# Kernel optimization log

Measured on AMD Instinct MI355X. Metric: run time of the kernel, lower is better.

Reference implementation:

```python
import jax, jax.numpy as jnp
import numpy as np

D_MODEL = 1024
N_EXPERTS = 16
TOP_K = 2
D_FF = 512      # per-expert SwiGLU hidden size
D_FF_SHARED = 1024
N_TOKENS = 4096


def setup_inputs() -> dict:
    key = jax.random.key(0)
    ks = jax.random.split(key, 9)
    s_in = 1.0 / np.sqrt(D_MODEL)
    s_ff = 1.0 / np.sqrt(D_FF)
    s_fs = 1.0 / np.sqrt(D_FF_SHARED)
    return {
        "hidden_states": jax.random.normal(ks[0], (N_TOKENS, D_MODEL), jnp.float32),
        "Wg": jax.random.normal(ks[1], (D_MODEL, N_EXPERTS), jnp.float32) * s_in,
        "w1": jax.random.normal(ks[2], (N_EXPERTS, D_MODEL, D_FF), jnp.float32) * s_in,
        "w3": jax.random.normal(ks[3], (N_EXPERTS, D_MODEL, D_FF), jnp.float32) * s_in,
        "w2": jax.random.normal(ks[4], (N_EXPERTS, D_FF, D_MODEL), jnp.float32) * s_ff,
        "ws1": jax.random.normal(ks[5], (D_MODEL, D_FF_SHARED), jnp.float32) * s_in,
        "ws3": jax.random.normal(ks[6], (D_MODEL, D_FF_SHARED), jnp.float32) * s_in,
        "ws2": jax.random.normal(ks[7], (D_FF_SHARED, D_MODEL), jnp.float32) * s_fs,
        "capacity": 1024,
    }


def reference(hidden_states, Wg, w1, w3, w2, ws1, ws3, ws2, capacity):
    T, d = hidden_states.shape
    E = Wg.shape[1]
    C = capacity

    # --- router: softmax in fp32, top-k, renormalize (norm_topk_prob=True) ---
    logits = hidden_states @ Wg                                  # [T, E]
    probs = jax.nn.softmax(logits.astype(jnp.float32), axis=-1)
    topw, topi = jax.lax.top_k(probs, TOP_K)                     # [T, K]
    topw = topw / jnp.sum(topw, axis=-1, keepdims=True)
    topw = topw.astype(hidden_states.dtype)

    # --- dispatch: flatten (token, k) pairs, compute slot within expert buffer ---
    flat_e = topi.reshape(-1)                                    # [T*K] expert id
    flat_t = jnp.repeat(jnp.arange(T), TOP_K)                    # [T*K] source token
    flat_w = topw.reshape(-1)                                    # [T*K]
    oh = jax.nn.one_hot(flat_e, E, dtype=jnp.int32)              # [T*K, E]
    # exclusive position of each pair within its expert's buffer
    pos = jnp.sum((jnp.cumsum(oh, axis=0) - 1) * oh, axis=-1)    # [T*K]
    keep = pos < C
    slot = jnp.where(keep, flat_e * C + pos, E * C)              # dropped -> dummy row

    buf = jnp.zeros((E * C + 1, d), hidden_states.dtype)
    buf = buf.at[slot].set(hidden_states[flat_t])
    xb = buf[: E * C].reshape(E, C, d)                           # [E, C, d]

    # --- per-expert SwiGLU MLP (grouped matmuls) ---
    h = jax.nn.silu(jnp.einsum("ecd,edf->ecf", xb, w1)) * jnp.einsum("ecd,edf->ecf", xb, w3)
    ob = jnp.einsum("ecf,efd->ecd", h, w2).reshape(E * C, d)     # [E*C, d]

    # --- weighted combine: gather expert outputs, scatter-add into token rows ---
    gathered = ob[jnp.minimum(slot, E * C - 1)]                  # [T*K, d]
    y = gathered * (flat_w * keep.astype(flat_w.dtype))[:, None]
    final = jnp.zeros_like(hidden_states).at[flat_t].add(y)

    # --- shared expert (dense SwiGLU over all tokens) ---
    sh = jax.nn.silu(hidden_states @ ws1) * (hidden_states @ ws3)
    final = final + sh @ ws2
    return final
```

## Files before the change

### kernel.cpp

```cpp
#include <hip/hip_runtime.h>
#include <stdint.h>

#define TT 4096
#define DM 1024
#define NE 16
#define DFF 512
#define DFS 1024
#define CAP 1024

typedef unsigned short u16;
typedef __bf16 bf16x8 __attribute__((ext_vector_type(8)));
typedef float f32x4 __attribute__((ext_vector_type(4)));

typedef __attribute__((address_space(1))) void as1_void;
typedef __attribute__((address_space(3))) void as3_void;

__device__ __forceinline__ u16 f2bf(float f) {
  union { float f; uint32_t u; } v; v.f = f;
  uint32_t u = v.u;
  u += 0x7fffu + ((u >> 16) & 1u);
  return (u16)(u >> 16);
}

__device__ __forceinline__ float bf2f(u16 b) {
  union { uint32_t u; float f; } v; v.u = ((uint32_t)b) << 16;
  return v.f;
}

__device__ __forceinline__ void gl2lds16(const void* g, void* l) {
  __builtin_amdgcn_global_load_lds(
      (as1_void*)(uintptr_t)g,
      (as3_void*)(uint32_t)(uintptr_t)l,
      16, 0, 0);
}

__global__ __launch_bounds__(256) void k_prep(
    const float* __restrict__ x, const float* __restrict__ Wg,
    const float* __restrict__ w1, const float* __restrict__ w3,
    const float* __restrict__ w2, const float* __restrict__ ws1,
    const float* __restrict__ ws3, const float* __restrict__ ws2,
    u16* __restrict__ hbf,
    u16* __restrict__ w1t, u16* __restrict__ w3t, u16* __restrict__ w2t,
    u16* __restrict__ ws1t, u16* __restrict__ ws3t, u16* __restrict__ ws2t,
    int* __restrict__ counts, int* __restrict__ tok_slot,
    int* __restrict__ tslot, float* __restrict__ tw) {
  __shared__ __align__(16) char smraw[18624];
  const int bid = blockIdx.x;
  const int tid = threadIdx.x;

  if (bid < 256) {
    float (*red)[16][17] = (float(*)[16][17])smraw;
    float (*lg)[17] = (float(*)[17])(smraw + 17408);
    int tl = tid >> 4, kp = tid & 15;
    int t = bid * 16 + tl;
    const float* xr = x + (size_t)t * DM + kp * 64;
    u16* hr = hbf + (size_t)t * DM + kp * 64;
    float acc[16];
#pragma unroll
    for (int e = 0; e < 16; ++e) acc[e] = 0.f;
#pragma unroll 4
    for (int i = 0; i < 16; ++i) {
      float4 xv = *(const float4*)(xr + i * 4);
      ushort4 o;
      o.x = f2bf(xv.x); o.y = f2bf(xv.y); o.z = f2bf(xv.z); o.w = f2bf(xv.w);
      *(ushort4*)(hr + i * 4) = o;
      const float* wgr = Wg + (size_t)(kp * 64 + i * 4) * NE;
#pragma unroll
      for (int q = 0; q < 4; ++q) {
        float xq = (q == 0) ? xv.x : (q == 1) ? xv.y : (q == 2) ? xv.z : xv.w;
        float4 a = *(const float4*)(wgr + q * NE);
        float4 b = *(const float4*)(wgr + q * NE + 4);
        float4 c = *(const float4*)(wgr + q * NE + 8);
        float4 d = *(const float4*)(wgr + q * NE + 12);
        acc[0] += xq * a.x;  acc[1] += xq * a.y;  acc[2] += xq * a.z;  acc[3] += xq * a.w;
        acc[4] += xq * b.x;  acc[5] += xq * b.y;  acc[6] += xq * b.z;  acc[7] += xq * b.w;
        acc[8] += xq * c.x;  acc[9] += xq * c.y;  acc[10] += xq * c.z; acc[11] += xq * c.w;
        acc[12] += xq * d.x; acc[13] += xq * d.y; acc[14] += xq * d.z; acc[15] += xq * d.w;
      }
    }
#pragma unroll
    for (int e = 0; e < 16; ++e) red[tl][kp][e] = acc[e];
    __syncthreads();
    float logit = 0.f;
#pragma unroll
    for (int p = 0; p < 16; ++p) logit += red[tl][p][kp];
    lg[tl][kp] = logit;
    __syncthreads();
    if (kp == 0) {
      float b0 = -1e30f; int i0 = 0;
#pragma unroll
      for (int i = 0; i < NE; ++i) { float v = lg[tl][i]; if (v > b0) { b0 = v; i0 = i; } }
      float b1 = -1e30f; int i1 = 0;
#pragma unroll
      for (int i = 0; i < NE; ++i) { if (i == i0) continue; float v = lg[tl][i]; if (v > b1) { b1 = v; i1 = i; } }
      float ex = __expf(b1 - b0);
      float w0 = 1.f / (1.f + ex);
      float w1v = 1.f - w0;
      int p0 = atomicAdd(&counts[i0], 1);
      int s0 = -1;
      if (p0 < CAP) { s0 = i0 * CAP + p0; tok_slot[s0] = t; }
      tslot[2 * t] = s0; tw[2 * t] = w0;
      int p1 = atomicAdd(&counts[i1], 1);
      int s1 = -1;
      if (p1 < CAP) { s1 = i1 * CAP + p1; tok_slot[s1] = t; }
      tslot[2 * t + 1] = s1; tw[2 * t + 1] = w1v;
    }
    return;
  }

  int tb = bid - 256;
  const float* ip; u16* op; int R, C, rt, ct;
  if (tb < 6144) {
    int slice = tb >> 7, ti = tb & 127;
    if (slice < 16)      { ip = w1 + (size_t)slice * DM * DFF; op = w1t + (size_t)slice * DM * DFF; R = DM;  C = DFF; rt = ti >> 3; ct = ti & 7; }
    else if (slice < 32) { int e = slice - 16; ip = w3 + (size_t)e * DM * DFF; op = w3t + (size_t)e * DM * DFF; R = DM;  C = DFF; rt = ti >> 3; ct = ti & 7; }
    else                 { int e = slice - 32; ip = w2 + (size_t)e * DFF * DM; op = w2t + (size_t)e * DFF * DM; R = DFF; C = DM;  rt = ti >> 4; ct = ti & 15; }
  } else {
    int tb2 = tb - 6144; int slice = tb2 >> 8, ti = tb2 & 255;
    if (slice == 0)      { ip = ws1; op = ws1t; }
    else if (slice == 1) { ip = ws3; op = ws3t; }
    else                 { ip = ws2; op = ws2t; }
    R = 1024; C = 1024; rt = ti >> 4; ct = ti & 15;
  }
  int r0 = rt * 64, c0 = ct * 64;

  float* tile = (float*)smraw;
  int tx = tid & 15, ty = tid >> 4;
#pragma unroll
  for (int j = 0; j < 4; ++j) {
    int r = ty + 16 * j;
    float4 v = *(const float4*)&ip[(size_t)(r0 + r) * C + c0 + tx * 4];
    int base = r * 64;
    int cc = tx * 4;
    tile[base + ((cc + 0 + r) & 63)] = v.x;
    tile[base + ((cc + 1 + r) & 63)] = v.y;
    tile[base + ((cc + 2 + r) & 63)] = v.z;
    tile[base + ((cc + 3 + r) & 63)] = v.w;
  }
  __syncthreads();
#pragma unroll
  for (int j = 0; j < 4; ++j) {
    int c = ty + 16 * j;
    int rr = tx * 4;
    ushort4 o;
    o.x = f2bf(tile[(rr + 0) * 64 + ((c + rr + 0) & 63)]);
    o.y = f2bf(tile[(rr + 1) * 64 + ((c + rr + 1) & 63)]);
    o.z = f2bf(tile[(rr + 2) * 64 + ((c + rr + 2) & 63)]);
    o.w = f2bf(tile[(rr + 3) * 64 + ((c + rr + 3) & 63)]);
    *(ushort4*)&op[(size_t)(c0 + c) * R + r0 + rr] = o;
  }
}

#define FRAG(BUF, ROW, CC)                                                       \
  (*(const bf16x8*)&BUF[(ROW) * 64 + ((((CC) * 4 + lq) ^ ((ROW) & 7)) << 3)])

__global__ __launch_bounds__(128) void k_up(
    const u16* __restrict__ hbf,
    const u16* __restrict__ ws1t, const u16* __restrict__ ws3t,
    const u16* __restrict__ w1t, const u16* __restrict__ w3t,
    u16* __restrict__ hs, u16* __restrict__ hexp,
    const int* __restrict__ counts, const int* __restrict__ tok_slot) {
  const int bid = blockIdx.x;
  const int tid = threadIdx.x;
  const u16* B1p; const u16* B3p; u16* Cp;
  int m0, n0, N;
  int e = -1, cnt = 0;
  if (bid < 512) {
    m0 = (bid >> 4) * 128; n0 = (bid & 15) * 64;
    B1p = ws1t; B3p = ws3t; Cp = hs; N = DFS;
  } else {
    int r = bid - 512;
    e = r >> 6; int q = r & 63;
    m0 = (q >> 3) * 128; n0 = (q & 7) * 64;
    cnt = counts[e]; if (cnt > CAP) cnt = CAP;
    if (m0 >= cnt) return;
    B1p = w1t + (size_t)e * (DFF * DM);
    B3p = w3t + (size_t)e * (DFF * DM);
    Cp = hexp + (size_t)e * (CAP * DFF);
    N = DFF;
  }

  __shared__ __align__(16) u16 As[128 * 64];
  __shared__ __align__(16) u16 Bs1[64 * 64];
  __shared__ __align__(16) u16 Bs3[64 * 64];

  uint32_t aoff[8], boff[4];
#pragma unroll
  for (int j = 0; j < 8; ++j) {
    int L = tid + 128 * j;
    int row = L >> 3;
    int c = (L & 7) ^ (row & 7);
    int gr;
    if (e >= 0) {
      int rr = m0 + row;
      gr = (rr < cnt) ? tok_slot[e * CAP + rr] : 0;
    } else {
      gr = m0 + row;
    }
    aoff[j] = (uint32_t)gr * DM + c * 8;
  }
#pragma unroll
  for (int j = 0; j < 4; ++j) {
    int L = tid + 128 * j;
    int row = L >> 3;
    int c = (L & 7) ^ (row & 7);
    boff[j] = (uint32_t)(n0 + row) * DM + c * 8;
  }

  const int lane = tid & 63;
  const int wv = tid >> 6;
  const int wr = wv * 64;
  const int lr = lane & 15;
  const int lq = lane >> 4;

  f32x4 acc1[4][4], acc3[4][4];
#pragma unroll
  for (int i = 0; i < 4; ++i)
#pragma unroll
    for (int j = 0; j < 4; ++j) {
      acc1[i][j] = (f32x4){0.f, 0.f, 0.f, 0.f};
      acc3[i][j] = (f32x4){0.f, 0.f, 0.f, 0.f};
    }

  for (int k0 = 0; k0 < DM; k0 += 64) {
    __syncthreads();
#pragma unroll
    for (int j = 0; j < 8; ++j) gl2lds16(hbf + aoff[j] + k0, &As[(size_t)(tid + 128 * j) * 8]);
#pragma unroll
    for (int j = 0; j < 4; ++j) gl2lds16(B1p + boff[j] + k0, &Bs1[(size_t)(tid + 128 * j) * 8]);
#pragma unroll
    for (int j = 0; j < 4; ++j) gl2lds16(B3p + boff[j] + k0, &Bs3[(size_t)(tid + 128 * j) * 8]);
    __syncthreads();
#pragma unroll
    for (int cc = 0; cc < 2; ++cc) {
      bf16x8 af[4], bf1[4], bf3[4];
#pragma unroll
      for (int i = 0; i < 4; ++i) af[i] = FRAG(As, wr + i * 16 + lr, cc);
#pragma unroll
      for (int j = 0; j < 4; ++j) {
        bf1[j] = FRAG(Bs1, j * 16 + lr, cc);
        bf3[j] = FRAG(Bs3, j * 16 + lr, cc);
      }
#pragma unroll
      for (int i = 0; i < 4; ++i)
#pragma unroll
        for (int j = 0; j < 4; ++j) {
          acc1[i][j] = __builtin_amdgcn_mfma_f32_16x16x32_bf16(af[i], bf1[j], acc1[i][j], 0, 0, 0);
          acc3[i][j] = __builtin_amdgcn_mfma_f32_16x16x32_bf16(af[i], bf3[j], acc3[i][j], 0, 0, 0);
        }
    }
  }

#pragma unroll
  for (int i = 0; i < 4; ++i)
#pragma unroll
    for (int r = 0; r < 4; ++r) {
      int row = m0 + wr + i * 16 + lq * 4 + r;
      u16* crow = Cp + (size_t)row * N;
#pragma unroll
      for (int j = 0; j < 4; ++j) {
        float v1 = acc1[i][j][r];
        float v3 = acc3[i][j][r];
        float h = (v1 / (1.f + __expf(-v1))) * v3;
        crow[n0 + j * 16 + lr] = f2bf(h);
      }
    }
}

__global__ __launch_bounds__(128) void k_down(
    const u16* __restrict__ hs, const u16* __restrict__ ws2t,
    const u16* __restrict__ hexp, const u16* __restrict__ w2t,
    float* __restrict__ out, u16* __restrict__ ob,
    const int* __restrict__ counts) {
  const int bid = blockIdx.x;
  const int tid = threadIdx.x;
  const u16* Ap; const u16* Bp;
  int m0, n0, K, e = -1;
  if (bid < 512) {
    m0 = (bid >> 4) * 128; n0 = (bid & 15) * 64;
    Ap = hs; Bp = ws2t; K = DFS;
  } else {
    int r = bid - 512;
    e = r >> 7; int q = r & 127;
    m0 = (q >> 4) * 128; n0 = (q & 15) * 64;
    int cnt = counts[e]; if (cnt > CAP) cnt = CAP;
    if (m0 >= cnt) return;
    Ap = hexp + (size_t)e * (CAP * DFF);
    Bp = w2t + (size_t)e * (DM * DFF);
    K = DFF;
  }

  __shared__ __align__(16) u16 As[128 * 64];
  __shared__ __align__(16) u16 Bs[64 * 64];

  uint32_t aoff[8], boff[4];
#pragma unroll
  for (int j = 0; j < 8; ++j) {
    int L = tid + 128 * j;
    int row = L >> 3;
    int c = (L & 7) ^ (row & 7);
    aoff[j] = (uint32_t)(m0 + row) * K + c * 8;
  }
#pragma unroll
  for (int j = 0; j < 4; ++j) {
    int L = tid + 128 * j;
    int row = L >> 3;
    int c = (L & 7) ^ (row & 7);
    boff[j] = (uint32_t)(n0 + row) * K + c * 8;
  }

  const int lane = tid & 63;
  const int wv = tid >> 6;
  const int wr = wv * 64;
  const int lr = lane & 15;
  const int lq = lane >> 4;

  f32x4 acc[4][4];
#pragma unroll
  for (int i = 0; i < 4; ++i)
#pragma unroll
    for (int j = 0; j < 4; ++j) acc[i][j] = (f32x4){0.f, 0.f, 0.f, 0.f};

  for (int k0 = 0; k0 < K; k0 += 64) {
    __syncthreads();
#pragma unroll
    for (int j = 0; j < 8; ++j) gl2lds16(Ap + aoff[j] + k0, &As[(size_t)(tid + 128 * j) * 8]);
#pragma unroll
    for (int j = 0; j < 4; ++j) gl2lds16(Bp + boff[j] + k0, &Bs[(size_t)(tid + 128 * j) * 8]);
    __syncthreads();
#pragma unroll
    for (int cc = 0; cc < 2; ++cc) {
      bf16x8 af[4], bfr[4];
#pragma unroll
      for (int i = 0; i < 4; ++i) af[i] = FRAG(As, wr + i * 16 + lr, cc);
#pragma unroll
      for (int j = 0; j < 4; ++j) bfr[j] = FRAG(Bs, j * 16 + lr, cc);
#pragma unroll
      for (int i = 0; i < 4; ++i)
#pragma unroll
        for (int j = 0; j < 4; ++j)
          acc[i][j] = __builtin_amdgcn_mfma_f32_16x16x32_bf16(af[i], bfr[j], acc[i][j], 0, 0, 0);
    }
  }

  if (e < 0) {
#pragma unroll
    for (int i = 0; i < 4; ++i)
#pragma unroll
      for (int r = 0; r < 4; ++r) {
        int row = m0 + wr + i * 16 + lq * 4 + r;
        float* orow = out + (size_t)row * DM;
#pragma unroll
        for (int j = 0; j < 4; ++j)
          orow[n0 + j * 16 + lr] = acc[i][j][r];
      }
  } else {
    u16* obase = ob + (size_t)e * CAP * DM;
#pragma unroll
    for (int i = 0; i < 4; ++i)
#pragma unroll
      for (int r = 0; r < 4; ++r) {
        int row = m0 + wr + i * 16 + lq * 4 + r;
        u16* orow = obase + (size_t)row * DM;
#pragma unroll
        for (int j = 0; j < 4; ++j)
          orow[n0 + j * 16 + lr] = f2bf(acc[i][j][r]);
      }
  }
}

__global__ __launch_bounds__(256) void k_combine(
    float* __restrict__ out, const u16* __restrict__ ob,
    const int* __restrict__ tslot, const float* __restrict__ tw) {
  int t = blockIdx.x;
  int c = threadIdx.x * 4;
  int s0 = tslot[2 * t], s1 = tslot[2 * t + 1];
  float w0 = tw[2 * t], w1 = tw[2 * t + 1];
  float4 v = *(float4*)&out[(size_t)t * DM + c];
  if (s0 >= 0) {
    ushort4 o = *(const ushort4*)&ob[(size_t)s0 * DM + c];
    v.x += w0 * bf2f(o.x); v.y += w0 * bf2f(o.y);
    v.z += w0 * bf2f(o.z); v.w += w0 * bf2f(o.w);
  }
  if (s1 >= 0) {
    ushort4 o = *(const ushort4*)&ob[(size_t)s1 * DM + c];
    v.x += w1 * bf2f(o.x); v.y += w1 * bf2f(o.y);
    v.z += w1 * bf2f(o.z); v.w += w1 * bf2f(o.w);
  }
  *(float4*)&out[(size_t)t * DM + c] = v;
}

extern "C" void kernel_launch(void* const* d_in, const int* in_sizes, int n_in,
                              void* d_out, int out_size, void* d_ws, size_t ws_size,
                              hipStream_t stream) {
  (void)in_sizes; (void)n_in; (void)out_size; (void)ws_size;
  const float* x   = (const float*)d_in[0];
  const float* Wg  = (const float*)d_in[1];
  const float* w1  = (const float*)d_in[2];
  const float* w3  = (const float*)d_in[3];
  const float* w2  = (const float*)d_in[4];
  const float* ws1 = (const float*)d_in[5];
  const float* ws3 = (const float*)d_in[6];
  const float* ws2 = (const float*)d_in[7];
  float* out = (float*)d_out;
  char* ws = (char*)d_ws;

  u16* hbf   = (u16*)(ws + 0);
  u16* w1t   = (u16*)(ws + 8388608);
  u16* w3t   = (u16*)(ws + 25165824);
  u16* w2t   = (u16*)(ws + 41943040);
  u16* ws1t  = (u16*)(ws + 58720256);
  u16* ws3t  = (u16*)(ws + 60817408);
  u16* ws2t  = (u16*)(ws + 62914560);
  u16* hs    = (u16*)(ws + 65011712);
  u16* hexp  = (u16*)(ws + 73400320);
  int* counts    = (int*)(ws + 90177536);
  int* tok_slot  = (int*)(ws + 90177792);
  int* tslot     = (int*)(ws + 90243328);
  float* tw      = (float*)(ws + 90276096);
  u16* ob    = (u16*)(ws + 0);

  hipMemsetAsync(counts, 0, NE * sizeof(int), stream);

  k_prep<<<dim3(256 + 6912), dim3(256), 0, stream>>>(
      x, Wg, w1, w3, w2, ws1, ws3, ws2,
      hbf, w1t, w3t, w2t, ws1t, ws3t, ws2t,
      counts, tok_slot, tslot, tw);

  k_up<<<dim3(512 + NE * 64), dim3(128), 0, stream>>>(
      hbf, ws1t, ws3t, w1t, w3t, hs, hexp, counts, tok_slot);

  k_down<<<dim3(512 + NE * 128), dim3(128), 0, stream>>>(
      hs, ws2t, hexp, w2t, out, ob, counts);

  k_combine<<<dim3(TT), dim3(256), 0, stream>>>(out, ob, tslot, tw);
}
```

Measured before the change: 342.7 us.

## Use 128x128 tiles with 4 waves, BK=32, and XCD-aware expert mapping

Both grouped GEMM kernels move from 128x64 tiles with 2 waves and BK=64 to 128x128 tiles with 4 waves (2x2) and BK=32, using a new LDS swizzle for the 32-wide K slices. Expert blocks are remapped so that each XCD handles two experts, which should keep that expert's weights in the local L2. The larger N tile cuts how often A is re-read, and the smaller LDS footprint allows higher occupancy. In exchange there are twice as many K iterations, each with two barriers, and fewer blocks in flight for the shared GEMM.

```diff
diff --git a/kernel.cpp b/kernel.cpp
--- a/kernel.cpp
+++ b/kernel.cpp
@@ -151,10 +151,15 @@
   }
 }
 
-#define FRAG(BUF, ROW, CC)                                                       \
-  (*(const bf16x8*)&BUF[(ROW) * 64 + ((((CC) * 4 + lq) ^ ((ROW) & 7)) << 3)])
-
-__global__ __launch_bounds__(128) void k_up(
+#define FRAG32(BUF, ROW)                                                          \
+  (*(const bf16x8*)&BUF[((ROW) >> 1) * 64 +                                       \
+                        ((((((ROW) & 1) * 4 + lq) ^ (((ROW) >> 1) & 7)) << 3))])
+
+#define STAGE_DECODE(L, ROW, KC)                                                  \
+  { int _l = (L) >> 3; int _c = ((L) & 7) ^ (_l & 7);                             \
+    ROW = 2 * _l + (_c >> 2); KC = (_c & 3) * 8; }
+
+__global__ __launch_bounds__(256, 4) void k_up(
     const u16* __restrict__ hbf,
     const u16* __restrict__ ws1t, const u16* __restrict__ ws3t,
     const u16* __restrict__ w1t, const u16* __restrict__ w3t,
@@ -165,13 +170,15 @@
   const u16* B1p; const u16* B3p; u16* Cp;
   int m0, n0, N;
   int e = -1, cnt = 0;
-  if (bid < 512) {
-    m0 = (bid >> 4) * 128; n0 = (bid & 15) * 64;
+  if (bid < 256) {
+    m0 = (bid >> 3) * 128; n0 = (bid & 7) * 128;
     B1p = ws1t; B3p = ws3t; Cp = hs; N = DFS;
   } else {
-    int r = bid - 512;
-    e = r >> 6; int q = r & 63;
-    m0 = (q >> 3) * 128; n0 = (q & 7) * 64;
+    int r = bid - 256;
+    int xcd = r & 7, p = r >> 3;
+    e = xcd * 2 + (p >> 5);
+    int q = p & 31;
+    m0 = (q >> 2) * 128; n0 = (q & 3) * 128;
     cnt = counts[e]; if (cnt > CAP) cnt = CAP;
     if (m0 >= cnt) return;
     B1p = w1t + (size_t)e * (DFF * DM);
@@ -180,16 +187,16 @@
     N = DFF;
   }
 
-  __shared__ __align__(16) u16 As[128 * 64];
-  __shared__ __align__(16) u16 Bs1[64 * 64];
-  __shared__ __align__(16) u16 Bs3[64 * 64];
-
-  uint32_t aoff[8], boff[4];
-#pragma unroll
-  for (int j = 0; j < 8; ++j) {
-    int L = tid + 128 * j;
-    int row = L >> 3;
-    int c = (L & 7) ^ (row & 7);
+  __shared__ __align__(16) u16 As[128 * 32];
+  __shared__ __align__(16) u16 Bs1[128 * 32];
+  __shared__ __align__(16) u16 Bs3[128 * 32];
+
+  uint32_t aoff[2], boff[2];
+#pragma unroll
+  for (int j = 0; j < 2; ++j) {
+    int L = tid + 256 * j;
+    int row, kc;
+    STAGE_DECODE(L, row, kc);
     int gr;
     if (e >= 0) {
       int rr = m0 + row;
@@ -197,19 +204,14 @@
     } else {
       gr = m0 + row;
     }
-    aoff[j] = (uint32_t)gr * DM + c * 8;
-  }
-#pragma unroll
-  for (int j = 0; j < 4; ++j) {
-    int L = tid + 128 * j;
-    int row = L >> 3;
-    int c = (L & 7) ^ (row & 7);
-    boff[j] = (uint32_t)(n0 + row) * DM + c * 8;
+    aoff[j] = (uint32_t)gr * DM + kc;
+    boff[j] = (uint32_t)(n0 + row) * DM + kc;
   }
 
   const int lane = tid & 63;
   const int wv = tid >> 6;
-  const int wr = wv * 64;
+  const int wr = (wv >> 1) * 64;
+  const int wc = (wv & 1) * 64;
   const int lr = lane & 15;
   const int lq = lane >> 4;
 
@@ -222,33 +224,30 @@
       acc3[i][j] = (f32x4){0.f, 0.f, 0.f, 0.f};
     }
 
-  for (int k0 = 0; k0 < DM; k0 += 64) {
-    __syncthreads();
-#pragma unroll
-    for (int j = 0; j < 8; ++j) gl2lds16(hbf + aoff[j] + k0, &As[(size_t)(tid + 128 * j) * 8]);
-#pragma unroll
-    for (int j = 0; j < 4; ++j) gl2lds16(B1p + boff[j] + k0, &Bs1[(size_t)(tid + 128 * j) * 8]);
-#pragma unroll
-    for (int j = 0; j < 4; ++j) gl2lds16(B3p + boff[j] + k0, &Bs3[(size_t)(tid + 128 * j) * 8]);
-    __syncthreads();
-#pragma unroll
-    for (int cc = 0; cc < 2; ++cc) {
-      bf16x8 af[4], bf1[4], bf3[4];
-#pragma unroll
-      for (int i = 0; i < 4; ++i) af[i] = FRAG(As, wr + i * 16 + lr, cc);
+  for (int k0 = 0; k0 < DM; k0 += 32) {
+    __syncthreads();
+#pragma unroll
+    for (int j = 0; j < 2; ++j) gl2lds16(hbf + aoff[j] + k0, &As[(size_t)(tid + 256 * j) * 8]);
+#pragma unroll
+    for (int j = 0; j < 2; ++j) gl2lds16(B1p + boff[j] + k0, &Bs1[(size_t)(tid + 256 * j) * 8]);
+#pragma unroll
+    for (int j = 0; j < 2; ++j) gl2lds16(B3p + boff[j] + k0, &Bs3[(size_t)(tid + 256 * j) * 8]);
+    __syncthreads();
+    bf16x8 af[4], bf1[4], bf3[4];
+#pragma unroll
+    for (int i = 0; i < 4; ++i) af[i] = FRAG32(As, wr + i * 16 + lr);
+#pragma unroll
+    for (int j = 0; j < 4; ++j) {
+      bf1[j] = FRAG32(Bs1, wc + j * 16 + lr);
+      bf3[j] = FRAG32(Bs3, wc + j * 16 + lr);
+    }
+#pragma unroll
+    for (int i = 0; i < 4; ++i)
 #pragma unroll
       for (int j = 0; j < 4; ++j) {
-        bf1[j] = FRAG(Bs1, j * 16 + lr, cc);
-        bf3[j] = FRAG(Bs3, j * 16 + lr, cc);
+        acc1[i][j] = __builtin_amdgcn_mfma_f32_16x16x32_bf16(af[i], bf1[j], acc1[i][j], 0, 0, 0);
+        acc3[i][j] = __builtin_amdgcn_mfma_f32_16x16x32_bf16(af[i], bf3[j], acc3[i][j], 0, 0, 0);
       }
-#pragma unroll
-      for (int i = 0; i < 4; ++i)
-#pragma unroll
-        for (int j = 0; j < 4; ++j) {
-          acc1[i][j] = __builtin_amdgcn_mfma_f32_16x16x32_bf16(af[i], bf1[j], acc1[i][j], 0, 0, 0);
-          acc3[i][j] = __builtin_amdgcn_mfma_f32_16x16x32_bf16(af[i], bf3[j], acc3[i][j], 0, 0, 0);
-        }
-    }
   }
 
 #pragma unroll
@@ -262,12 +261,12 @@
         float v1 = acc1[i][j][r];
         float v3 = acc3[i][j][r];
         float h = (v1 / (1.f + __expf(-v1))) * v3;
-        crow[n0 + j * 16 + lr] = f2bf(h);
+        crow[n0 + wc + j * 16 + lr] = f2bf(h);
       }
     }
 }
 
-__global__ __launch_bounds__(128) void k_down(
+__global__ __launch_bounds__(256, 4) void k_down(
     const u16* __restrict__ hs, const u16* __restrict__ ws2t,
     const u16* __restrict__ hexp, const u16* __restrict__ w2t,
     float* __restrict__ out, u16* __restrict__ ob,
@@ -276,13 +275,15 @@
   const int tid = threadIdx.x;
   const u16* Ap; const u16* Bp;
   int m0, n0, K, e = -1;
-  if (bid < 512) {
-    m0 = (bid >> 4) * 128; n0 = (bid & 15) * 64;
+  if (bid < 256) {
+    m0 = (bid >> 3) * 128; n0 = (bid & 7) * 128;
     Ap = hs; Bp = ws2t; K = DFS;
   } else {
-    int r = bid - 512;
-    e = r >> 7; int q = r & 127;
-    m0 = (q >> 4) * 128; n0 = (q & 15) * 64;
+    int r = bid - 256;
+    int xcd = r & 7, p = r >> 3;
+    e = xcd * 2 + (p >> 6);
+    int q = p & 63;
+    m0 = (q >> 3) * 128; n0 = (q & 7) * 128;
     int cnt = counts[e]; if (cnt > CAP) cnt = CAP;
     if (m0 >= cnt) return;
     Ap = hexp + (size_t)e * (CAP * DFF);
@@ -290,28 +291,23 @@
     K = DFF;
   }
 
-  __shared__ __align__(16) u16 As[128 * 64];
-  __shared__ __align__(16) u16 Bs[64 * 64];
-
-  uint32_t aoff[8], boff[4];
-#pragma unroll
-  for (int j = 0; j < 8; ++j) {
-    int L = tid + 128 * j;
-    int row = L >> 3;
-    int c = (L & 7) ^ (row & 7);
-    aoff[j] = (uint32_t)(m0 + row) * K + c * 8;
-  }
-#pragma unroll
-  for (int j = 0; j < 4; ++j) {
-    int L = tid + 128 * j;
-    int row = L >> 3;
-    int c = (L & 7) ^ (row & 7);
-    boff[j] = (uint32_t)(n0 + row) * K + c * 8;
+  __shared__ __align__(16) u16 As[128 * 32];
+  __shared__ __align__(16) u16 Bs[128 * 32];
+
+  uint32_t aoff[2], boff[2];
+#pragma unroll
+  for (int j = 0; j < 2; ++j) {
+    int L = tid + 256 * j;
+    int row, kc;
+    STAGE_DECODE(L, row, kc);
+    aoff[j] = (uint32_t)(m0 + row) * K + kc;
+    boff[j] = (uint32_t)(n0 + row) * K + kc;
   }
 
   const int lane = tid & 63;
   const int wv = tid >> 6;
-  const int wr = wv * 64;
+  const int wr = (wv >> 1) * 64;
+  const int wc = (wv & 1) * 64;
   const int lr = lane & 15;
   const int lq = lane >> 4;
 
@@ -321,26 +317,23 @@
 #pragma unroll
     for (int j = 0; j < 4; ++j) acc[i][j] = (f32x4){0.f, 0.f, 0.f, 0.f};
 
-  for (int k0 = 0; k0 < K; k0 += 64) {
-    __syncthreads();
-#pragma unroll
-    for (int j = 0; j < 8; ++j) gl2lds16(Ap + aoff[j] + k0, &As[(size_t)(tid + 128 * j) * 8]);
-#pragma unroll
-    for (int j = 0; j < 4; ++j) gl2lds16(Bp + boff[j] + k0, &Bs[(size_t)(tid + 128 * j) * 8]);
-    __syncthreads();
-#pragma unroll
-    for (int cc = 0; cc < 2; ++cc) {
-      bf16x8 af[4], bfr[4];
-#pragma unroll
-      for (int i = 0; i < 4; ++i) af[i] = FRAG(As, wr + i * 16 + lr, cc);
-#pragma unroll
-      for (int j = 0; j < 4; ++j) bfr[j] = FRAG(Bs, j * 16 + lr, cc);
-#pragma unroll
-      for (int i = 0; i < 4; ++i)
-#pragma unroll
-        for (int j = 0; j < 4; ++j)
-          acc[i][j] = __builtin_amdgcn_mfma_f32_16x16x32_bf16(af[i], bfr[j], acc[i][j], 0, 0, 0);
-    }
+  for (int k0 = 0; k0 < K; k0 += 32) {
+    __syncthreads();
+#pragma unroll
+    for (int j = 0; j < 2; ++j) gl2lds16(Ap + aoff[j] + k0, &As[(size_t)(tid + 256 * j) * 8]);
+#pragma unroll
+    for (int j = 0; j < 2; ++j) gl2lds16(Bp + boff[j] + k0, &Bs[(size_t)(tid + 256 * j) * 8]);
+    __syncthreads();
+    bf16x8 af[4], bfr[4];
+#pragma unroll
+    for (int i = 0; i < 4; ++i) af[i] = FRAG32(As, wr + i * 16 + lr);
+#pragma unroll
+    for (int j = 0; j < 4; ++j) bfr[j] = FRAG32(Bs, wc + j * 16 + lr);
+#pragma unroll
+    for (int i = 0; i < 4; ++i)
+#pragma unroll
+      for (int j = 0; j < 4; ++j)
+        acc[i][j] = __builtin_amdgcn_mfma_f32_16x16x32_bf16(af[i], bfr[j], acc[i][j], 0, 0, 0);
   }
 
   if (e < 0) {
@@ -352,7 +345,7 @@
         float* orow = out + (size_t)row * DM;
 #pragma unroll
         for (int j = 0; j < 4; ++j)
-          orow[n0 + j * 16 + lr] = acc[i][j][r];
+          orow[n0 + wc + j * 16 + lr] = acc[i][j][r];
       }
   } else {
     u16* obase = ob + (size_t)e * CAP * DM;
@@ -364,7 +357,7 @@
         u16* orow = obase + (size_t)row * DM;
 #pragma unroll
         for (int j = 0; j < 4; ++j)
-          orow[n0 + j * 16 + lr] = f2bf(acc[i][j][r]);
+          orow[n0 + wc + j * 16 + lr] = f2bf(acc[i][j][r]);
       }
   }
 }
@@ -427,10 +420,10 @@
       hbf, w1t, w3t, w2t, ws1t, ws3t, ws2t,
       counts, tok_slot, tslot, tw);
 
-  k_up<<<dim3(512 + NE * 64), dim3(128), 0, stream>>>(
+  k_up<<<dim3(256 + 512), dim3(256), 0, stream>>>(
       hbf, ws1t, ws3t, w1t, w3t, hs, hexp, counts, tok_slot);
 
-  k_down<<<dim3(512 + NE * 128), dim3(128), 0, stream>>>(
+  k_down<<<dim3(256 + 1024), dim3(256), 0, stream>>>(
       hs, ws2t, hexp, w2t, out, ob, counts);
 
   k_combine<<<dim3(TT), dim3(256), 0, stream>>>(out, ob, tslot, tw);
```

Measured after the change: 664.4 us. 93.9% more time.
